# Optimization experiments

Hardware: AMD Instinct MI355X
Metric: run time of the kernel (lower is better)

## Reference

```python
import jax, jax.numpy as jnp
import numpy as np

M, K, N = 4096, 4096, 16384  # tokens, input_size, output_size


def setup_inputs() -> dict:
    key = jax.random.key(0)
    k_x, k_w, k_s, k_b = jax.random.split(key, 4)
    x = jax.random.normal(k_x, (M, K), dtype=jnp.float32)
    # Pre-quantized int8 weight, [output_size, input_size] layout as stored by QuantizedLinear.
    weight_q = jax.random.randint(k_w, (N, K), -127, 128, dtype=jnp.int8)
    # Per-channel (per-output) dequant scale; positive, realistic magnitude ~ 2/127.
    weight_scale = (jax.random.uniform(k_s, (N,), dtype=jnp.float32) + 0.5) * (2.0 / 127.0)
    bias = jax.random.normal(k_b, (N,), dtype=jnp.float32)
    return {"x": x, "weight_q": weight_q, "weight_scale": weight_scale, "bias": bias}


def reference(x, weight_q, weight_scale, bias):
    """QuantizedLinear.__call__ with activation_dtype=None, sequence_parallel=False.

    xla_quantized_matmul_local: cast int8 weight to compute dtype, GEMM against x,
    apply per-output-channel weight_scale after the matmul, then add bias.
    weight_q is [N, K]; contraction is x[m,k] * w[n,k] -> out[m,n].
    """
    w = weight_q.astype(jnp.float32)
    out = jnp.einsum("mk,nk->mn", x, w, preferred_element_type=jnp.float32)
    out = out * weight_scale[None, :]  # per-channel dequant
    return out + bias[None, :]
```

## Files before the change

### kernel.cpp

```cpp
#include <hip/hip_runtime.h>


static constexpr int Mdim = 4096;
static constexpr int Kdim = 4096;
static constexpr int Ndim = 16384;

static constexpr int BM = 128, BN = 128, BK = 64;
static constexpr int TILES_N = Ndim / BN;
static constexpr int TILES_M = Mdim / BM;

static constexpr int BM2 = 256, BN2 = 256, BK2 = 64;
static constexpr int TM2 = Mdim / BM2;
static constexpr int TN2 = Ndim / BN2;
static constexpr int NT2 = Kdim / BK2;
static constexpr int NWG2 = TM2 * TN2;

typedef __attribute__((ext_vector_type(8))) short bf16x8;
typedef __attribute__((ext_vector_type(4))) float f32x4;

__device__ __forceinline__ unsigned packbf(float lo, float hi) {
  unsigned a = __builtin_bit_cast(unsigned, lo);
  unsigned b = __builtin_bit_cast(unsigned, hi);
  a += 0x7FFFu + ((a >> 16) & 1u);
  b += 0x7FFFu + ((b >> 16) & 1u);
  return (a >> 16) | (b & 0xFFFF0000u);
}

__device__ __forceinline__ unsigned i32x2bf(int lo, int hi) {
  float f0 = (float)lo;
  float f1 = (float)hi;
  return (__builtin_bit_cast(unsigned, f0) >> 16) |
         (__builtin_bit_cast(unsigned, f1) & 0xFFFF0000u);
}

__global__ void cvt_x_kernel(const float4* __restrict__ in, uint4* __restrict__ out) {
  int i = blockIdx.x * 256 + threadIdx.x;
  float4 a = in[2 * i];
  float4 b = in[2 * i + 1];
  uint4 o;
  o.x = packbf(a.x, a.y);
  o.y = packbf(a.z, a.w);
  o.z = packbf(b.x, b.y);
  o.w = packbf(b.z, b.w);
  out[i] = o;
}

__global__ void cvt_w_kernel(const int4* __restrict__ in, uint4* __restrict__ out) {
  int i = blockIdx.x * 256 + threadIdx.x;
  int4 a = in[2 * i];
  int4 b = in[2 * i + 1];
  uint4 o;
  o.x = i32x2bf(a.x, a.y);
  o.y = i32x2bf(a.z, a.w);
  o.z = i32x2bf(b.x, b.y);
  o.w = i32x2bf(b.z, b.w);
  out[i] = o;
}


__global__ __launch_bounds__(512, 2) void gemm_bf16_8ph(
    const unsigned short* __restrict__ A,
    const unsigned short* __restrict__ B,
    const float* __restrict__ scale,
    const float* __restrict__ bias,
    float* __restrict__ out) {
  __shared__ unsigned short As[2 * 2 * 1024 * 8];
  __shared__ unsigned short Bs[2 * 2 * 1024 * 8];

  const int tid = threadIdx.x;
  const int lane = tid & 63;
  const int w = tid >> 6;
  const int wm = w >> 2;
  const int wn = w & 3;
  const int l15 = lane & 15;
  const int quad = lane >> 4;
  const int sw = l15 & 7;
  const int bhalf = wn >> 1;

  const int bid = blockIdx.x;
  const int wg = (bid & 7) * (NWG2 / 8) + (bid >> 3);
  const int bm = wg / TN2, bn = wg % TN2;
  const int row0 = bm * BM2, col0 = bn * BN2;

  unsigned aoff[2][2], boff[2][2];
#pragma unroll
  for (int h = 0; h < 2; ++h)
#pragma unroll
    for (int i = 0; i < 2; ++i) {
      int ch = (w * 2 + i) * 64 + lane;
      int ir = ch >> 3;
      int c = (ch & 7) ^ (ir & 7);
      int ra = (ir >> 6) * 128 + h * 64 + (ir & 63);
      int rb = h * 128 + ir;
      aoff[h][i] = (unsigned)((((long)(row0 + ra)) * Kdim + c * 8) * 2);
      boff[h][i] = (unsigned)((((long)(col0 + rb)) * Kdim + c * 8) * 2);
    }

#define STG_A(d, h, kt)                                                                   \
  do {                                                                                    \
    __builtin_amdgcn_global_load_lds(                                                     \
        (const __attribute__((address_space(1))) void*)((const char*)A + aoff[h][0] + (kt)*128), \
        (__attribute__((address_space(3))) void*)(&As[(((d)*2 + (h)) * 1024 + (w*2 + 0) * 64) * 8]), 16, 0, 0); \
    __builtin_amdgcn_global_load_lds(                                                     \
        (const __attribute__((address_space(1))) void*)((const char*)A + aoff[h][1] + (kt)*128), \
        (__attribute__((address_space(3))) void*)(&As[(((d)*2 + (h)) * 1024 + (w*2 + 1) * 64) * 8]), 16, 0, 0); \
  } while (0)

#define STG_B(d, h, kt)                                                                   \
  do {                                                                                    \
    __builtin_amdgcn_global_load_lds(                                                     \
        (const __attribute__((address_space(1))) void*)((const char*)B + boff[h][0] + (kt)*128), \
        (__attribute__((address_space(3))) void*)(&Bs[(((d)*2 + (h)) * 1024 + (w*2 + 0) * 64) * 8]), 16, 0, 0); \
    __builtin_amdgcn_global_load_lds(                                                     \
        (const __attribute__((address_space(1))) void*)((const char*)B + boff[h][1] + (kt)*128), \
        (__attribute__((address_space(3))) void*)(&Bs[(((d)*2 + (h)) * 1024 + (w*2 + 1) * 64) * 8]), 16, 0, 0); \
  } while (0)

#define LDA(dst, d, h, t3, ks)                                                            \
  dst = *(const bf16x8*)(As + ((((d)*2 + (h)) * 1024 + (wm * 64 + (t3) * 16 + l15) * 8 +  \
                                (((ks)*4 + quad) ^ sw)) * 8))
#define LDB(dst, d, n, ks)                                                                \
  dst = *(const bf16x8*)(Bs + ((((d)*2 + bhalf) * 1024 + ((wn & 1) * 64 + (n) * 16 + l15) * 8 + \
                                (((ks)*4 + quad) ^ sw)) * 8))

#define LDA8(d, h)                                                                        \
  _Pragma("unroll") for (int t = 0; t < 4; ++t) {                                         \
    LDA(af[t][0], d, h, t, 0);                                                            \
    LDA(af[t][1], d, h, t, 1);                                                            \
  }

#define LDB2(d, n0)                                                                       \
  _Pragma("unroll") for (int n = 0; n < 2; ++n) {                                         \
    LDB(bf[n][0], d, (n0) + n, 0);                                                        \
    LDB(bf[n][1], d, (n0) + n, 1);                                                        \
  }

#define MFMAQ(mb, nb)                                                                     \
  __builtin_amdgcn_s_setprio(1);                                                          \
  _Pragma("unroll") for (int mi = 0; mi < 4; ++mi) {                                      \
    _Pragma("unroll") for (int ni = 0; ni < 2; ++ni) {                                    \
      _Pragma("unroll") for (int ks = 0; ks < 2; ++ks) {                                  \
        acc[(mb) + mi][(nb) + ni] = __builtin_amdgcn_mfma_f32_16x16x32_bf16(              \
            af[mi][ks], bf[ni][ks], acc[(mb) + mi][(nb) + ni], 0, 0, 0);                  \
      }                                                                                   \
    }                                                                                     \
  }                                                                                       \
  __builtin_amdgcn_s_setprio(0);

#define BAR __builtin_amdgcn_s_barrier()
#define LGKM0 asm volatile("s_waitcnt lgkmcnt(0)" ::: "memory")
#define VMC(n) asm volatile("s_waitcnt vmcnt(" #n ")" ::: "memory")

#define GROUP(g, d, dn, S1, S2)              \
  {                                          \
    LDA8(d, 0);                              \
    LDB2(d, 0);                              \
    if (S1) STG_A(dn, 0, (g) + 1);           \
    BAR;                                     \
    LGKM0;                                   \
    MFMAQ(0, 0);                             \
    BAR;                                     \
    LDA8(d, 1);                              \
    if (S1) STG_B(dn, 1, (g) + 1);           \
    BAR;                                     \
    LGKM0;                                   \
    MFMAQ(4, 0);                             \
    BAR;                                     \
    LDB2(d, 2);                              \
    if (S2) STG_A(d, 1, (g) + 2);            \
    BAR;                                     \
    LGKM0;                                   \
    MFMAQ(4, 2);                             \
    BAR;                                     \
    LDA8(d, 0);                              \
    if (S2) STG_B(d, 0, (g) + 2);            \
    BAR;                                     \
    LGKM0;                                   \
    MFMAQ(0, 2);                             \
    VMC(4);                                  \
    BAR;                                     \
  }

  f32x4 acc[8][4];
#pragma unroll
  for (int mi = 0; mi < 8; ++mi)
#pragma unroll
    for (int ni = 0; ni < 4; ++ni) acc[mi][ni] = (f32x4){0.f, 0.f, 0.f, 0.f};

  bf16x8 af[4][2];
  bf16x8 bf[2][2];

  STG_A(0, 0, 0);
  STG_A(0, 1, 0);
  STG_B(0, 0, 0);
  STG_B(0, 1, 0);
  STG_A(1, 1, 1);
  STG_B(1, 0, 1);
  VMC(4);
  BAR;

#pragma unroll 1
  for (int g = 0; g < NT2 - 2; g += 2) {
    GROUP(g, 0, 1, 1, 1);
    GROUP(g + 1, 1, 0, 1, 1);
  }
  GROUP(NT2 - 2, 0, 1, 1, 0);
  VMC(0);
  BAR;
  GROUP(NT2 - 1, 1, 0, 0, 0);

#undef GROUP
#undef STG_A
#undef STG_B
#undef LDA
#undef LDB
#undef LDA8
#undef LDB2
#undef MFMAQ

  const int rbase = quad * 4;
#pragma unroll
  for (int ni = 0; ni < 4; ++ni) {
    const int n = col0 + wn * 64 + ni * 16 + l15;
    const float sc = scale[n];
    const float bz = bias[n];
#pragma unroll
    for (int mi = 0; mi < 8; ++mi) {
      const int m = row0 + wm * 128 + mi * 16 + rbase;
      float* o = out + (long)m * Ndim + n;
#pragma unroll
      for (int r = 0; r < 4; ++r) o[(long)r * Ndim] = acc[mi][ni][r] * sc + bz;
    }
  }
}

__device__ __forceinline__ void mfma_tile(const unsigned short* As, const unsigned short* Bs,
                                          int am, int bnl, int quad, f32x4 acc[4][4]) {
#pragma unroll
  for (int ks = 0; ks < 2; ++ks) {
    const int c = ks * 4 + quad;
    bf16x8 af[4], bv[4];
#pragma unroll
    for (int t = 0; t < 4; ++t) {
      int ma = am + t * 16;
      af[t] = *(const bf16x8*)(As + (ma * 8 + (c ^ (ma & 7))) * 8);
      int nb = bnl + t * 16;
      bv[t] = *(const bf16x8*)(Bs + (nb * 8 + (c ^ (nb & 7))) * 8);
    }
#pragma unroll
    for (int mi = 0; mi < 4; ++mi)
#pragma unroll
      for (int ni = 0; ni < 4; ++ni)
        acc[mi][ni] = __builtin_amdgcn_mfma_f32_16x16x32_bf16(af[mi], bv[ni], acc[mi][ni], 0, 0, 0);
  }
}

__device__ __forceinline__ void epilogue128(float* __restrict__ out,
                                            const float* __restrict__ scale,
                                            const float* __restrict__ bias,
                                            int row0, int col0, int wm, int wn, int lane,
                                            f32x4 acc[4][4]) {
  const int rbase = (lane >> 4) * 4;
#pragma unroll
  for (int ni = 0; ni < 4; ++ni) {
    const int n = col0 + wn * 64 + ni * 16 + (lane & 15);
    const float sc = scale[n];
    const float bz = bias[n];
#pragma unroll
    for (int mi = 0; mi < 4; ++mi) {
      const int m = row0 + wm * 64 + mi * 16 + rbase;
      float* o = out + (long)m * Ndim + n;
#pragma unroll
      for (int r = 0; r < 4; ++r)
        o[(long)r * Ndim] = acc[mi][ni][r] * sc + bz;
    }
  }
}

__global__ __launch_bounds__(256, 2) void gemm_fused(const float* __restrict__ X,
                                                     const int* __restrict__ Wq,
                                                     const float* __restrict__ scale,
                                                     const float* __restrict__ bias,
                                                     float* __restrict__ out) {
  __shared__ unsigned short As[BM * BK];
  __shared__ unsigned short Bs[BN * BK];

  const int tid = threadIdx.x;
  const int lane = tid & 63;
  const int w = tid >> 6;
  const int wm = w & 1, wn = w >> 1;
  const int bid = blockIdx.x;
  const int bn = bid % TILES_N;
  const int bm = bid / TILES_N;
  const int row0 = bm * BM, col0 = bn * BN;

  int slot[4];
  long aoff[4], boff[4];
#pragma unroll
  for (int i = 0; i < 4; ++i) {
    int s = i * 256 + tid;
    int m = s >> 3, cs = s & 7, c = cs ^ (m & 7);
    slot[i] = s;
    aoff[i] = (long)(row0 + m) * Kdim + c * 8;
    boff[i] = (long)(col0 + m) * Kdim + c * 8;
  }

  f32x4 acc[4][4];
#pragma unroll
  for (int mi = 0; mi < 4; ++mi)
#pragma unroll
    for (int ni = 0; ni < 4; ++ni) acc[mi][ni] = (f32x4){0.f, 0.f, 0.f, 0.f};

  const int am = wm * 64 + (lane & 15);
  const int bnl = wn * 64 + (lane & 15);
  const int quad = lane >> 4;

  for (int kt = 0; kt < Kdim / BK; ++kt) {
    uint4 aw[4], bw[4];
#pragma unroll
    for (int i = 0; i < 4; ++i) {
      const float4* ap = (const float4*)(X + aoff[i] + kt * BK);
      float4 a0 = ap[0];
      float4 a1 = ap[1];
      aw[i].x = packbf(a0.x, a0.y);
      aw[i].y = packbf(a0.z, a0.w);
      aw[i].z = packbf(a1.x, a1.y);
      aw[i].w = packbf(a1.z, a1.w);
      const int4* bp = (const int4*)(Wq + boff[i] + kt * BK);
      int4 b0 = bp[0];
      int4 b1 = bp[1];
      bw[i].x = i32x2bf(b0.x, b0.y);
      bw[i].y = i32x2bf(b0.z, b0.w);
      bw[i].z = i32x2bf(b1.x, b1.y);
      bw[i].w = i32x2bf(b1.z, b1.w);
    }
    __syncthreads();
#pragma unroll
    for (int i = 0; i < 4; ++i) {
      *(uint4*)(&As[slot[i] * 8]) = aw[i];
      *(uint4*)(&Bs[slot[i] * 8]) = bw[i];
    }
    __syncthreads();
    mfma_tile(As, Bs, am, bnl, quad, acc);
  }
  epilogue128(out, scale, bias, row0, col0, wm, wn, lane, acc);
}

extern "C" void kernel_launch(void* const* d_in, const int* in_sizes, int n_in,
                              void* d_out, int out_size, void* d_ws, size_t ws_size,
                              hipStream_t stream) {
  const float* x = (const float*)d_in[0];
  const int* wq = (const int*)d_in[1];
  const float* wscale = (const float*)d_in[2];
  const float* wbias = (const float*)d_in[3];
  float* out = (float*)d_out;

  const size_t needA = ((size_t)Mdim * Kdim + (size_t)Ndim * Kdim) * 2;
  if (ws_size >= needA) {
    unsigned short* xb = (unsigned short*)d_ws;
    unsigned short* wb = xb + (size_t)Mdim * Kdim;
    cvt_x_kernel<<<(Mdim * Kdim) / 8 / 256, 256, 0, stream>>>((const float4*)x, (uint4*)xb);
    cvt_w_kernel<<<(Ndim / 256) * (Kdim / 8), 256, 0, stream>>>((const int4*)wq, (uint4*)wb);
    gemm_bf16_8ph<<<NWG2, 512, 0, stream>>>(xb, wb, wscale, wbias, out);
  } else {
    gemm_fused<<<TILES_M * TILES_N, 256, 0, stream>>>(x, wq, wscale, wbias, out);
  }
}
```

Before: 1.178 ms.

## Reorder K-tile prefetch schedule and issue MFMAs via inline asm with AGPR accumulators

Restructures the per-group pipeline so B tiles for the next K-step are prefetched together early and A tiles two steps ahead, changing the quadrant order of MFMA blocks to reuse loaded fragments. The MFMA loop is reordered to iterate ks outermost and emitted as inline asm with accumulators pinned to AGPRs, intended to reduce register pressure and give better MFMA issue back-to-back. The change risks LDS hazards from the new staging order and compiler scheduling losses from opaque asm.

New measurement: 1.091 ms. 1.08x faster.

```diff
diff --git a/kernel.cpp b/kernel.cpp
--- a/kernel.cpp
+++ b/kernel.cpp
@@ -137,11 +137,12 @@
 
 #define MFMAQ(mb, nb)                                                                     \
   __builtin_amdgcn_s_setprio(1);                                                          \
-  _Pragma("unroll") for (int mi = 0; mi < 4; ++mi) {                                      \
-    _Pragma("unroll") for (int ni = 0; ni < 2; ++ni) {                                    \
-      _Pragma("unroll") for (int ks = 0; ks < 2; ++ks) {                                  \
-        acc[(mb) + mi][(nb) + ni] = __builtin_amdgcn_mfma_f32_16x16x32_bf16(              \
-            af[mi][ks], bf[ni][ks], acc[(mb) + mi][(nb) + ni], 0, 0, 0);                  \
+  _Pragma("unroll") for (int ks = 0; ks < 2; ++ks) {                                      \
+    _Pragma("unroll") for (int mi = 0; mi < 4; ++mi) {                                    \
+      _Pragma("unroll") for (int ni = 0; ni < 2; ++ni) {                                  \
+        asm("v_mfma_f32_16x16x32_bf16 %0, %1, %2, %0"                                     \
+            : "+a"(acc[(mb) + mi][(nb) + ni])                                             \
+            : "v"(af[mi][ks]), "v"(bf[ni][ks]));                                          \
       }                                                                                   \
     }                                                                                     \
   }                                                                                       \
@@ -151,33 +152,35 @@
 #define LGKM0 asm volatile("s_waitcnt lgkmcnt(0)" ::: "memory")
 #define VMC(n) asm volatile("s_waitcnt vmcnt(" #n ")" ::: "memory")
 
-#define GROUP(g, d, dn, S1, S2)              \
+#define GROUP(g, d, dn, SB, SA, V)           \
   {                                          \
     LDA8(d, 0);                              \
     LDB2(d, 0);                              \
-    if (S1) STG_A(dn, 0, (g) + 1);           \
     BAR;                                     \
     LGKM0;                                   \
     MFMAQ(0, 0);                             \
     BAR;                                     \
+    LDB2(d, 2);                              \
+    if (SB) {                                \
+      STG_B(dn, 0, (g) + 1);                 \
+      STG_B(dn, 1, (g) + 1);                 \
+    }                                        \
+    BAR;                                     \
+    LGKM0;                                   \
+    MFMAQ(0, 2);                             \
+    BAR;                                     \
     LDA8(d, 1);                              \
-    if (S1) STG_B(dn, 1, (g) + 1);           \
+    if (SA) STG_A(d, 0, (g) + 2);            \
+    BAR;                                     \
+    LGKM0;                                   \
+    MFMAQ(4, 2);                             \
+    BAR;                                     \
+    LDB2(d, 0);                              \
+    if (SA) STG_A(d, 1, (g) + 2);            \
     BAR;                                     \
     LGKM0;                                   \
     MFMAQ(4, 0);                             \
-    BAR;                                     \
-    LDB2(d, 2);                              \
-    if (S2) STG_A(d, 1, (g) + 2);            \
-    BAR;                                     \
-    LGKM0;                                   \
-    MFMAQ(4, 2);                             \
-    BAR;                                     \
-    LDA8(d, 0);                              \
-    if (S2) STG_B(d, 0, (g) + 2);            \
-    BAR;                                     \
-    LGKM0;                                   \
-    MFMAQ(0, 2);                             \
-    VMC(4);                                  \
+    VMC(V);                                  \
     BAR;                                     \
   }
 
@@ -194,20 +197,18 @@
   STG_A(0, 1, 0);
   STG_B(0, 0, 0);
   STG_B(0, 1, 0);
+  STG_A(1, 0, 1);
   STG_A(1, 1, 1);
-  STG_B(1, 0, 1);
   VMC(4);
   BAR;
 
 #pragma unroll 1
   for (int g = 0; g < NT2 - 2; g += 2) {
-    GROUP(g, 0, 1, 1, 1);
-    GROUP(g + 1, 1, 0, 1, 1);
-  }
-  GROUP(NT2 - 2, 0, 1, 1, 0);
-  VMC(0);
-  BAR;
-  GROUP(NT2 - 1, 1, 0, 0, 0);
+    GROUP(g, 0, 1, 1, 1, 4);
+    GROUP(g + 1, 1, 0, 1, 1, 4);
+  }
+  GROUP(NT2 - 2, 0, 1, 1, 0, 0);
+  GROUP(NT2 - 1, 1, 0, 0, 0, 0);
 
 #undef GROUP
 #undef STG_A
```
